# Kernel tuning notes

Hardware: AMD Instinct MI355X
Metric: run time of the kernel (lower is better)

The kernel has to match this reference:

```python
import jax, jax.numpy as jnp
import numpy as np

H = 16  # num_attention_heads


def setup_inputs() -> dict:
    key = jax.random.key(0)
    k1, k2, k3 = jax.random.split(key, 3)
    B, S, E = 2, 2048, 1024
    return {
        "hidden_states": jax.random.normal(k1, (B, S, E), dtype=jnp.float32),
        "W_attn": jax.random.normal(k2, (E, 3 * E), dtype=jnp.float32) * 0.02,
        "b_attn": jnp.zeros((3 * E,), dtype=jnp.float32),
        "W_proj": jax.random.normal(k3, (E, E), dtype=jnp.float32) * 0.02,
        "b_proj": jnp.zeros((E,), dtype=jnp.float32),
    }


def reference(hidden_states, W_attn, b_attn, W_proj, b_proj):
    B, S, E = hidden_states.shape
    hd = E // H
    # Conv1D: x @ W + b -> [B, S, 3E]
    qkv = hidden_states @ W_attn + b_attn
    # Faithful to module: _split_heads with 3*head_dim FIRST, then split q/k/v.
    # i.e. per-head slice of size 3*hd is [q_h | k_h | v_h] (interleaved layout).
    qkv = qkv.reshape(B, S, H, 3 * hd).transpose(0, 2, 1, 3)  # [B, H, S, 3*hd]
    q, k, v = jnp.split(qkv, 3, axis=-1)                      # each [B, H, S, hd]
    # scores, scaled by sqrt(head_dim) (value.size(-1) ** 0.5)
    scores = jnp.einsum("bhqd,bhkd->bhqk", q, k) / jnp.asarray(hd, q.dtype) ** 0.5
    # causal mask via where with masked_bias = -10000.0 (not -inf), as in module
    causal = jnp.tril(jnp.ones((S, S), dtype=bool))
    scores = jnp.where(causal, scores, jnp.asarray(-10000.0, scores.dtype))
    attn_weights = jax.nn.softmax(scores, axis=-1)  # dropout p=0 -> identity
    attn_out = jnp.einsum("bhqk,bhkd->bhqd", attn_weights, v)
    attn_out = attn_out.transpose(0, 2, 1, 3).reshape(B, S, E)  # merge heads
    return attn_out @ W_proj + b_proj
```

## Files before the change

### kernel.cpp

```cpp
#include <hip/hip_runtime.h>
#include <hip/hip_bf16.h>


typedef __attribute__((ext_vector_type(4))) float f32x4;
typedef __attribute__((ext_vector_type(16))) float f32x16;
typedef __attribute__((ext_vector_type(8))) short short8;
typedef __attribute__((ext_vector_type(2))) unsigned int uint2v;

#define AS1 __attribute__((address_space(1)))
#define AS3 __attribute__((address_space(3)))

__device__ __forceinline__ void load_lds16(const void* g, void* l) {
    __builtin_amdgcn_global_load_lds((const AS1 void*)g, (AS3 void*)l, 16, 0, 0);
}

__device__ __forceinline__ unsigned short f2bf(float f) {
    union { float f; unsigned int u; } v; v.f = f;
    unsigned int r = v.u + 0x7FFFu + ((v.u >> 16) & 1u);
    return (unsigned short)(r >> 16);
}

__device__ __forceinline__ int cvt_pk_bf16(float lo, float hi) {
    int r;
    asm("v_cvt_pk_bf16_f32 %0, %1, %2" : "=v"(r) : "v"(lo), "v"(hi));
    return r;
}

__device__ __forceinline__ float fexp2(float x) {
    float r;
    asm("v_exp_f32 %0, %1" : "=v"(r) : "v"(x));
    return r;
}

__device__ __forceinline__ void transpose_tile(
    const float* __restrict__ W, unsigned short* __restrict__ Wt,
    int K, int N, int bx, int by, int t) {
    __shared__ float tile[32][33];
    int k0 = by * 32, n0 = bx * 32;
    int r = t >> 3, c = (t & 7) * 4;
    float4 v = *(const float4*)&W[(size_t)(k0 + r) * N + n0 + c];
    tile[r][c] = v.x; tile[r][c + 1] = v.y; tile[r][c + 2] = v.z; tile[r][c + 3] = v.w;
    __syncthreads();
    int n = t >> 3; int kk = (t & 7) * 4;
    ushort4 o;
    o.x = f2bf(tile[kk + 0][n]);
    o.y = f2bf(tile[kk + 1][n]);
    o.z = f2bf(tile[kk + 2][n]);
    o.w = f2bf(tile[kk + 3][n]);
    *(ushort4*)&Wt[(size_t)(n0 + n) * K + k0 + kk] = o;
}

__global__ __launch_bounds__(256) void prep(
    const float* __restrict__ hs, unsigned short* __restrict__ Xb,
    const float* __restrict__ W_attn, unsigned short* __restrict__ WaT,
    const float* __restrict__ W_proj, unsigned short* __restrict__ WpT) {
    int bid = blockIdx.x, t = threadIdx.x;
    if (bid < 4096) {
        int i = (bid * 256 + t) * 4;
        float4 v = *(const float4*)(hs + i);
        ushort4 o;
        o.x = f2bf(v.x); o.y = f2bf(v.y); o.z = f2bf(v.z); o.w = f2bf(v.w);
        *(ushort4*)(Xb + i) = o;
    } else if (bid < 7168) {
        int r = bid - 4096;
        transpose_tile(W_attn, WaT, 1024, 3072, r % 96, r / 96, t);
    } else {
        int r = bid - 7168;
        transpose_tile(W_proj, WpT, 1024, 1024, r % 32, r / 32, t);
    }
}

__global__ __launch_bounds__(512, 6) void gemm_qkv(
    const unsigned short* __restrict__ A,
    const unsigned short* __restrict__ Bt,
    const float* __restrict__ bias,
    unsigned short* __restrict__ qk, unsigned short* __restrict__ Vt,
    int M, int N, int K) {
    __shared__ unsigned short Sh[2][8192];
    unsigned short* Tb = &Sh[0][0];
    const int t = threadIdx.x, wave = t >> 6, lane = t & 63;
    const int l15 = lane & 15, quad = lane >> 4;
    const int m0 = blockIdx.y * 128, n0 = blockIdx.x * 128;
    const int sw = wave & 3;
    const bool isB = wave >= 4;
    const int srow = sw * 32 + (lane >> 2);
    const int sch = (lane & 3) * 8;
    const unsigned short* G0 = isB ? (Bt + (size_t)(n0 + srow) * K + sch)
                                   : (A + (size_t)(m0 + srow) * K + sch);
    const int stOff = (isB ? 4096 : 0) + sw * 1024;
    const int wr = wave >> 1, wc = wave & 1;
    f32x4 acc[2][4] = {};
    const int NSTEP = K / 32;
    load_lds16(G0, &Sh[0][stOff]);
    load_lds16(G0 + (size_t)16 * K, &Sh[0][stOff + 512]);
    for (int kt = 0; kt < NSTEP; ++kt) {
        const int cur = kt & 1;
        const unsigned short* As = &Sh[cur][0];
        const unsigned short* Bs = &Sh[cur][4096];
        __syncthreads();
        if (kt + 1 < NSTEP) {
            const int k1 = (kt + 1) * 32;
            load_lds16(G0 + k1, &Sh[cur ^ 1][stOff]);
            load_lds16(G0 + k1 + (size_t)16 * K, &Sh[cur ^ 1][stOff + 512]);
        }
        short8 af[2], bf[4];
#pragma unroll
        for (int i = 0; i < 2; ++i)
            af[i] = *(const short8*)&As[(wr * 32 + i * 16 + l15) * 32 + quad * 8];
#pragma unroll
        for (int i = 0; i < 4; ++i)
            bf[i] = *(const short8*)&Bs[(wc * 64 + i * 16 + l15) * 32 + quad * 8];
        __builtin_amdgcn_s_setprio(1);
#pragma unroll
        for (int mt = 0; mt < 2; ++mt)
#pragma unroll
            for (int nt = 0; nt < 4; ++nt)
                acc[mt][nt] = __builtin_amdgcn_mfma_f32_16x16x32_bf16(af[mt], bf[nt], acc[mt][nt], 0, 0, 0);
        __builtin_amdgcn_s_setprio(0);
    }
    __syncthreads();
    const int rem = n0 % 192;
#pragma unroll
    for (int mt = 0; mt < 2; ++mt) {
        int mrow = m0 + wr * 32 + mt * 16 + quad * 4;
#pragma unroll
        for (int nt = 0; nt < 4; ++nt) {
            int col = n0 + wc * 64 + nt * 16 + l15;
            float bv = bias[col];
            int h = col / 192;
            int j = col - h * 192;
            if (j < 128) {
                float sc = (j < 64) ? 0.18033688011f : 1.0f;
#pragma unroll
                for (int r = 0; r < 4; ++r)
                    qk[(size_t)(mrow + r) * 2048 + h * 128 + j] = f2bf((acc[mt][nt][r] + bv) * sc);
            } else {
                int d = j - 128;
                int s_local = wr * 32 + mt * 16 + quad * 4;
                ushort4 pk;
                pk.x = f2bf(acc[mt][nt][0] + bv);
                pk.y = f2bf(acc[mt][nt][1] + bv);
                pk.z = f2bf(acc[mt][nt][2] + bv);
                pk.w = f2bf(acc[mt][nt][3] + bv);
                *(ushort4*)&Tb[d * 136 + s_local] = pk;
            }
        }
    }
    if (rem != 0) {
        __syncthreads();
        int vhalf = (rem == 64) ? 1 : 0;
        int h = (n0 + vhalf * 64) / 192;
        int b = m0 >> 11;
        unsigned short* vbase = Vt + ((size_t)(b * 16 + h) * 64) * 2048 + (m0 & 2047);
        int drow = t >> 4, ch = (t & 15) * 8;
#pragma unroll
        for (int rr = 0; rr < 2; ++rr) {
            int d = rr * 32 + drow;
            *(uint4*)(vbase + (size_t)d * 2048 + ch) = *(const uint4*)&Tb[d * 136 + ch];
        }
    }
}

__global__ __launch_bounds__(512, 4) void gemm_proj(
    const unsigned short* __restrict__ A,
    const unsigned short* __restrict__ Bt,
    const float* __restrict__ bias,
    float* __restrict__ C, int M, int N, int K) {
    __shared__ unsigned short Sh[2][6144];
    const int t = threadIdx.x, wave = t >> 6, lane = t & 63;
    const int l15 = lane & 15, quad = lane >> 4;
    const int m0 = blockIdx.y * 128, n0 = blockIdx.x * 64;
    const int sw = wave & 3;
    const bool isB = wave >= 4;
    const int srow = isB ? (sw * 16 + (lane >> 2)) : (sw * 32 + (lane >> 2));
    const int sch = (lane & 3) * 8;
    const unsigned short* G0 = isB ? (Bt + (size_t)(n0 + srow) * K + sch)
                                   : (A + (size_t)(m0 + srow) * K + sch);
    const int stOff = isB ? (4096 + sw * 512) : (sw * 1024);
    const int wr = wave >> 1, wc = wave & 1;
    f32x4 acc[2][2] = {};
    const int NSTEP = K / 32;
    load_lds16(G0, &Sh[0][stOff]);
    if (!isB) load_lds16(G0 + (size_t)16 * K, &Sh[0][stOff + 512]);
    for (int kt = 0; kt < NSTEP; ++kt) {
        const int cur = kt & 1;
        const unsigned short* As = &Sh[cur][0];
        const unsigned short* Bs = &Sh[cur][4096];
        __syncthreads();
        if (kt + 1 < NSTEP) {
            const int k1 = (kt + 1) * 32;
            load_lds16(G0 + k1, &Sh[cur ^ 1][stOff]);
            if (!isB) load_lds16(G0 + k1 + (size_t)16 * K, &Sh[cur ^ 1][stOff + 512]);
        }
        short8 af[2], bf[2];
#pragma unroll
        for (int i = 0; i < 2; ++i)
            af[i] = *(const short8*)&As[(wr * 32 + i * 16 + l15) * 32 + quad * 8];
#pragma unroll
        for (int i = 0; i < 2; ++i)
            bf[i] = *(const short8*)&Bs[(wc * 32 + i * 16 + l15) * 32 + quad * 8];
        __builtin_amdgcn_s_setprio(1);
#pragma unroll
        for (int mt = 0; mt < 2; ++mt)
#pragma unroll
            for (int nt = 0; nt < 2; ++nt)
                acc[mt][nt] = __builtin_amdgcn_mfma_f32_16x16x32_bf16(af[mt], bf[nt], acc[mt][nt], 0, 0, 0);
        __builtin_amdgcn_s_setprio(0);
    }
#pragma unroll
    for (int mt = 0; mt < 2; ++mt) {
        int mrow = m0 + wr * 32 + mt * 16 + quad * 4;
#pragma unroll
        for (int nt = 0; nt < 2; ++nt) {
            int col = n0 + wc * 32 + nt * 16 + l15;
            float bv = bias[col];
#pragma unroll
            for (int r = 0; r < 4; ++r)
                C[(size_t)(mrow + r) * N + col] = acc[mt][nt][r] + bv;
        }
    }
}

__global__ __launch_bounds__(512, 4) void attn6(
    const unsigned short* __restrict__ qk,
    const unsigned short* __restrict__ Vt,
    unsigned short* __restrict__ out) {
    const int S = 2048;
    __shared__ unsigned short Sh[2][16384];
    const int t = threadIdx.x, wave = t >> 6, lane = t & 63;
    const int l31 = lane & 31, half = lane >> 5;
    const int g = wave >> 2, gw = wave & 3;
    const int bid = blockIdx.x;
    const int qt = (bid < 256) ? (15 - (bid >> 5)) : ((bid - 256) >> 5);
    const int bh = bid & 31;
    const int b = bh >> 4, h = bh & 15;
    const unsigned short* qkb = qk + (size_t)b * S * 2048 + h * 128;
    const unsigned short* vtb = Vt + (size_t)bh * 64 * 2048;

    const int q0 = qt * 128 + gw * 32;
    short8 qf[4];
#pragma unroll
    for (int km = 0; km < 4; ++km)
        qf[km] = *(const short8*)(qkb + (size_t)(q0 + l31) * 2048 + km * 16 + half * 8);

    f32x16 o[2] = {};
    float lrun = 0.f;

    const int srow = t >> 3, c8 = t & 7;
    const int gsw = ((c8 ^ (srow & 7)) * 8);
    const int ldst = wave * 512;
    const unsigned short* kSrc = qkb + (size_t)srow * 2048 + 64 + gsw;
    const unsigned short* vSrc = vtb + (size_t)srow * 2048 + gsw;
    const int KTP = qt + 1;

    load_lds16(kSrc, &Sh[0][ldst]);
    load_lds16(kSrc + (size_t)64 * 2048, &Sh[0][4096 + ldst]);
    load_lds16(vSrc, &Sh[0][8192 + ldst]);
    load_lds16(vSrc + 64, &Sh[0][12288 + ldst]);

    const int qmax = q0 + 31;
    const int ksw = l31 & 7;
    int chs[4];
#pragma unroll
    for (int km = 0; km < 4; ++km)
        chs[km] = ((km * 2 + half) ^ ksw) * 8;
    const int krow = l31 * 64;
    const int gOff = g ? 4096 : 0;

    for (int p = 0; p < KTP; ++p) {
        const int cur = p & 1;
        __syncthreads();
        if (p + 1 < KTP) {
            const int k2 = (2 * p + 2) * 64;
            unsigned short* nb = &Sh[cur ^ 1][0];
            load_lds16(kSrc + (size_t)k2 * 2048, nb + ldst);
            load_lds16(kSrc + (size_t)(k2 + 64) * 2048, nb + 4096 + ldst);
            load_lds16(vSrc + k2, nb + 8192 + ldst);
            load_lds16(vSrc + k2 + 64, nb + 12288 + ldst);
        }
        const int kb = (2 * p + g) * 64;
        if (kb > qmax) continue;

        const unsigned short* Ksg = &Sh[cur][gOff];
        const unsigned short* Vsg = &Sh[cur][8192 + gOff];

        f32x16 s[2] = {};
        __builtin_amdgcn_s_setprio(1);
#pragma unroll
        for (int nt = 0; nt < 2; ++nt)
#pragma unroll
            for (int km = 0; km < 4; ++km) {
                short8 kf = *(const short8*)&Ksg[nt * 2048 + krow + chs[km]];
                s[nt] = __builtin_amdgcn_mfma_f32_32x32x16_bf16(kf, qf[km], s[nt], 0, 0, 0);
            }
        __builtin_amdgcn_s_setprio(0);

        if (kb + 63 > q0) {
#pragma unroll
            for (int nt = 0; nt < 2; ++nt)
#pragma unroll
                for (int r = 0; r < 16; ++r) {
                    int kg = kb + nt * 32 + (r & 3) + 8 * (r >> 2) + 4 * half;
                    if (kg > q0 + l31) s[nt][r] = -1e30f;
                }
        }

        int gd[2][4][2];
        float a0 = 0.f;
#pragma unroll
        for (int nt = 0; nt < 2; ++nt)
#pragma unroll
            for (int gg = 0; gg < 4; ++gg) {
                float e0 = fexp2(s[nt][4 * gg + 0]);
                float e1 = fexp2(s[nt][4 * gg + 1]);
                float e2 = fexp2(s[nt][4 * gg + 2]);
                float e3 = fexp2(s[nt][4 * gg + 3]);
                a0 += (e0 + e1) + (e2 + e3);
                gd[nt][gg][0] = cvt_pk_bf16(e0, e1);
                gd[nt][gg][1] = cvt_pk_bf16(e2, e3);
            }
        lrun += a0;

        short8 paf[4];
#pragma unroll
        for (int km = 0; km < 4; ++km) {
            const int nt = km >> 1, m = km & 1;
            uint2v w0 = __builtin_amdgcn_permlane32_swap(
                (unsigned)gd[nt][2 * m][0], (unsigned)gd[nt][2 * m + 1][0], false, false);
            uint2v w1 = __builtin_amdgcn_permlane32_swap(
                (unsigned)gd[nt][2 * m][1], (unsigned)gd[nt][2 * m + 1][1], false, false);
            int4 v = {(int)w0[0], (int)w1[0], (int)w0[1], (int)w1[1]};
            paf[km] = __builtin_bit_cast(short8, v);
        }

        __builtin_amdgcn_s_setprio(1);
#pragma unroll
        for (int nt2 = 0; nt2 < 2; ++nt2)
#pragma unroll
            for (int km = 0; km < 4; ++km) {
                short8 vf = *(const short8*)&Vsg[nt2 * 2048 + krow + chs[km]];
                o[nt2] = __builtin_amdgcn_mfma_f32_32x32x16_bf16(paf[km], vf, o[nt2], 0, 0, 0);
            }
        __builtin_amdgcn_s_setprio(0);
    }
    __syncthreads();

    float* Lf = (float*)&Sh[0][0];
    const int cidx = gw * 64 + lane;
    if (g == 1) {
        float* dst = Lf + cidx * 17;
#pragma unroll
        for (int r = 0; r < 16; ++r) dst[r] = o[0][r];
        dst[16] = lrun;
    }
    __syncthreads();
    float lsum = lrun;
    if (g == 0) {
        const float* src = Lf + cidx * 17;
#pragma unroll
        for (int r = 0; r < 16; ++r) o[0][r] += src[r];
        lsum += src[16];
    }
    __syncthreads();
    if (g == 1) {
        float* dst = Lf + cidx * 16;
#pragma unroll
        for (int r = 0; r < 16; ++r) dst[r] = o[1][r];
    }
    __syncthreads();
    if (g == 0) {
        const float* src = Lf + cidx * 16;
#pragma unroll
        for (int r = 0; r < 16; ++r) o[1][r] += src[r];
        float tot = lsum + __shfl_xor(lsum, 32);
        unsigned short* ob = out + (size_t)b * S * 1024 + h * 64;
#pragma unroll
        for (int r = 0; r < 16; ++r) {
            int ql = (r & 3) + 8 * (r >> 2) + 4 * half;
            float inv = 1.0f / __shfl(tot, ql);
            size_t row = (size_t)(q0 + ql) * 1024;
            ob[row + l31] = f2bf(o[0][r] * inv);
            ob[row + 32 + l31] = f2bf(o[1][r] * inv);
        }
    }
}

extern "C" void kernel_launch(void* const* d_in, const int* in_sizes, int n_in,
                              void* d_out, int out_size, void* d_ws, size_t ws_size,
                              hipStream_t stream) {
    const float* hs     = (const float*)d_in[0];
    const float* W_attn = (const float*)d_in[1];
    const float* b_attn = (const float*)d_in[2];
    const float* W_proj = (const float*)d_in[3];
    const float* b_proj = (const float*)d_in[4];
    float* out = (float*)d_out;

    const int B = 2, S = 2048, E = 1024;
    const int M = B * S;
    const int N3 = 3 * E;

    unsigned short* Xb  = (unsigned short*)d_ws;
    unsigned short* WaT = Xb + (size_t)M * E;
    unsigned short* WpT = WaT + (size_t)N3 * E;
    unsigned short* qkb = WpT + (size_t)E * E;
    unsigned short* Vt  = qkb + (size_t)M * 2048;
    unsigned short* ao  = Vt + (size_t)M * E;

    prep<<<dim3(8192), 256, 0, stream>>>(hs, Xb, W_attn, WaT, W_proj, WpT);

    gemm_qkv<<<dim3(N3 / 128, M / 128), 512, 0, stream>>>(Xb, WaT, b_attn, qkb, Vt, M, N3, E);

    attn6<<<dim3(512), 512, 0, stream>>>(qkb, Vt, ao);

    gemm_proj<<<dim3(E / 64, M / 128), 512, 0, stream>>>(ao, WpT, b_proj, out, M, E, E);
}
```

Baseline: 164.6 us.

## Triple-buffer LDS in QKV and projection GEMMs with explicit vmcnt waits

Both GEMM kernels move from double to triple buffering of LDS tiles. Loads are issued two k-steps ahead, and a partial s_waitcnt vmcnt plus a raw s_barrier replace __syncthreads. The aim is to hide global-to-LDS latency by keeping more loads in flight. It costs 50% more shared memory per block, which may lower occupancy, and correctness now depends on the hand-counted vmcnt values.

```diff
diff --git a/kernel.cpp b/kernel.cpp
--- a/kernel.cpp
+++ b/kernel.cpp
@@ -76,7 +76,7 @@
     const float* __restrict__ bias,
     unsigned short* __restrict__ qk, unsigned short* __restrict__ Vt,
     int M, int N, int K) {
-    __shared__ unsigned short Sh[2][8192];
+    __shared__ unsigned short Sh[3][8192];
     unsigned short* Tb = &Sh[0][0];
     const int t = threadIdx.x, wave = t >> 6, lane = t & 63;
     const int l15 = lane & 15, quad = lane >> 4;
@@ -91,18 +91,26 @@
     const int wr = wave >> 1, wc = wave & 1;
     f32x4 acc[2][4] = {};
     const int NSTEP = K / 32;
-    load_lds16(G0, &Sh[0][stOff]);
-    load_lds16(G0 + (size_t)16 * K, &Sh[0][stOff + 512]);
+#pragma unroll
+    for (int pb = 0; pb < 2; ++pb) {
+        const int kk = pb * 32;
+        load_lds16(G0 + kk, &Sh[pb][stOff]);
+        load_lds16(G0 + kk + (size_t)16 * K, &Sh[pb][stOff + 512]);
+    }
+    int cur = 0, stg = 2;
     for (int kt = 0; kt < NSTEP; ++kt) {
-        const int cur = kt & 1;
+        if (kt + 1 < NSTEP)
+            asm volatile("s_waitcnt vmcnt(2)" ::: "memory");
+        else
+            asm volatile("s_waitcnt vmcnt(0)" ::: "memory");
+        __builtin_amdgcn_s_barrier();
+        if (kt + 2 < NSTEP) {
+            const int k2 = (kt + 2) * 32;
+            load_lds16(G0 + k2, &Sh[stg][stOff]);
+            load_lds16(G0 + k2 + (size_t)16 * K, &Sh[stg][stOff + 512]);
+        }
         const unsigned short* As = &Sh[cur][0];
         const unsigned short* Bs = &Sh[cur][4096];
-        __syncthreads();
-        if (kt + 1 < NSTEP) {
-            const int k1 = (kt + 1) * 32;
-            load_lds16(G0 + k1, &Sh[cur ^ 1][stOff]);
-            load_lds16(G0 + k1 + (size_t)16 * K, &Sh[cur ^ 1][stOff + 512]);
-        }
         short8 af[2], bf[4];
 #pragma unroll
         for (int i = 0; i < 2; ++i)
@@ -117,6 +125,8 @@
             for (int nt = 0; nt < 4; ++nt)
                 acc[mt][nt] = __builtin_amdgcn_mfma_f32_16x16x32_bf16(af[mt], bf[nt], acc[mt][nt], 0, 0, 0);
         __builtin_amdgcn_s_setprio(0);
+        cur = (cur == 2) ? 0 : cur + 1;
+        stg = (stg == 2) ? 0 : stg + 1;
     }
     __syncthreads();
     const int rem = n0 % 192;
@@ -166,7 +176,7 @@
     const unsigned short* __restrict__ Bt,
     const float* __restrict__ bias,
     float* __restrict__ C, int M, int N, int K) {
-    __shared__ unsigned short Sh[2][6144];
+    __shared__ unsigned short Sh[3][6144];
     const int t = threadIdx.x, wave = t >> 6, lane = t & 63;
     const int l15 = lane & 15, quad = lane >> 4;
     const int m0 = blockIdx.y * 128, n0 = blockIdx.x * 64;
@@ -180,18 +190,28 @@
     const int wr = wave >> 1, wc = wave & 1;
     f32x4 acc[2][2] = {};
     const int NSTEP = K / 32;
-    load_lds16(G0, &Sh[0][stOff]);
-    if (!isB) load_lds16(G0 + (size_t)16 * K, &Sh[0][stOff + 512]);
+#pragma unroll
+    for (int pb = 0; pb < 2; ++pb) {
+        const int kk = pb * 32;
+        load_lds16(G0 + kk, &Sh[pb][stOff]);
+        if (!isB) load_lds16(G0 + kk + (size_t)16 * K, &Sh[pb][stOff + 512]);
+    }
+    int cur = 0, stg = 2;
     for (int kt = 0; kt < NSTEP; ++kt) {
-        const int cur = kt & 1;
+        if (kt + 1 < NSTEP) {
+            if (!isB) asm volatile("s_waitcnt vmcnt(2)" ::: "memory");
+            else      asm volatile("s_waitcnt vmcnt(1)" ::: "memory");
+        } else {
+            asm volatile("s_waitcnt vmcnt(0)" ::: "memory");
+        }
+        __builtin_amdgcn_s_barrier();
+        if (kt + 2 < NSTEP) {
+            const int k2 = (kt + 2) * 32;
+            load_lds16(G0 + k2, &Sh[stg][stOff]);
+            if (!isB) load_lds16(G0 + k2 + (size_t)16 * K, &Sh[stg][stOff + 512]);
+        }
         const unsigned short* As = &Sh[cur][0];
         const unsigned short* Bs = &Sh[cur][4096];
-        __syncthreads();
-        if (kt + 1 < NSTEP) {
-            const int k1 = (kt + 1) * 32;
-            load_lds16(G0 + k1, &Sh[cur ^ 1][stOff]);
-            if (!isB) load_lds16(G0 + k1 + (size_t)16 * K, &Sh[cur ^ 1][stOff + 512]);
-        }
         short8 af[2], bf[2];
 #pragma unroll
         for (int i = 0; i < 2; ++i)
@@ -206,6 +226,8 @@
             for (int nt = 0; nt < 2; ++nt)
                 acc[mt][nt] = __builtin_amdgcn_mfma_f32_16x16x32_bf16(af[mt], bf[nt], acc[mt][nt], 0, 0, 0);
         __builtin_amdgcn_s_setprio(0);
+        cur = (cur == 2) ? 0 : cur + 1;
+        stg = (stg == 2) ? 0 : stg + 1;
     }
 #pragma unroll
     for (int mt = 0; mt < 2; ++mt) {
```

Result: no change. 166.2 us (+1.0%).
